# Kernel tuning notes

Measured on AMD Instinct MI355X. Metric: run time of the kernel, lower is better.

Reference implementation:

```python
import jax, jax.numpy as jnp
import numpy as np

N = 6144
DIN1, DIN2, DOUT, NUM_HEADS = 3000, 512, 64, 8


@jax.custom_vjp
def _ms(x):
    # multispike forward: floor(clamp(x, 0, 4) + 0.5)
    return jnp.floor(jnp.clip(x, 0.0, 4.0) + 0.5)


def _ms_fwd(x):
    return _ms(x), x


def _ms_bwd(x, g):
    # surrogate gradient: pass-through on 0 < x < lens(=4)
    return (g * ((x > 0) & (x < 4)).astype(g.dtype),)


_ms.defvjp(_ms_fwd, _ms_bwd)


def spike(x):
    # Multispike module: spike(4*x)/4
    return _ms(4.0 * x) * 0.25


def _attn(x, wq, wk, wv, wp):
    # SpikeAttention: linear attention kv = k^T v, out = q @ kv * 0.25
    n, c = x.shape
    d = c // NUM_HEADS
    xs = spike(x)
    q = spike(xs @ wq).reshape(n, NUM_HEADS, d)
    k = spike(xs @ wk).reshape(n, NUM_HEADS, d)
    v = spike(xs @ wv).reshape(n, NUM_HEADS, d)
    kv = jnp.einsum('nhd,nhe->hde', k, v)          # [H, d, d]
    o = jnp.einsum('nhd,hde->nhe', q, kv) * 0.25    # [N, H, d]
    return o.reshape(n, c) @ wp


def _encoder(feat, adj, w, wq, wk, wv, wp):
    fe = feat @ w                 # feat embedding [N, DOUT]
    x = spike(adj @ fe)           # aggregate + spike
    return x + _attn(x, wq, wk, wv, wp)


def _decoder(emb, adj, w):
    return spike(adj @ (emb @ w))


def _xavier(k, shp):
    lim = float(np.sqrt(6.0 / (shp[0] + shp[1])))
    return jax.random.uniform(k, shp, jnp.float32, -lim, lim)


def setup_inputs() -> dict:
    key = jax.random.key(0)
    ks = jax.random.split(key, 26)
    inp = {}
    inp['features_omics1'] = jax.random.normal(ks[0], (N, DIN1), jnp.float32)
    inp['features_omics2'] = jax.random.normal(ks[1], (N, DIN2), jnp.float32)
    # dense normalized-ish adjacencies: entries ~ U(0, 2/N) so row sums ~ 1
    for i, nm in enumerate(['adj_spatial_omics1', 'adj_feature_omics1',
                            'adj_spatial_omics2', 'adj_feature_omics2']):
        inp[nm] = jax.random.uniform(ks[2 + i], (N, N), jnp.float32) * (2.0 / N)
    # 1x1 conv (Conv2dLSQ approximated as plain conv): weight [2], bias [1]
    inp['conv1_w'] = jax.random.normal(ks[6], (2,), jnp.float32) * 0.5
    inp['conv1_b'] = jnp.zeros((1,), jnp.float32)
    inp['conv2_w'] = jax.random.normal(ks[7], (2,), jnp.float32) * 0.5
    inp['conv2_b'] = jnp.zeros((1,), jnp.float32)
    inp['w_enc1'] = _xavier(ks[8], (DIN1, DOUT))
    inp['wq1'] = _xavier(ks[9], (DOUT, DOUT))
    inp['wk1'] = _xavier(ks[10], (DOUT, DOUT))
    inp['wv1'] = _xavier(ks[11], (DOUT, DOUT))
    inp['wp1'] = _xavier(ks[12], (DOUT, DOUT))
    inp['w_enc2'] = _xavier(ks[13], (DIN2, DOUT))
    inp['wq2'] = _xavier(ks[14], (DOUT, DOUT))
    inp['wk2'] = _xavier(ks[15], (DOUT, DOUT))
    inp['wv2'] = _xavier(ks[16], (DOUT, DOUT))
    inp['wp2'] = _xavier(ks[17], (DOUT, DOUT))
    inp['fc1_w'] = _xavier(ks[18], (2 * DOUT, DOUT))
    inp['fc1_b'] = jnp.zeros((DOUT,), jnp.float32)
    inp['fc2_w'] = _xavier(ks[19], (DOUT, DOUT))
    inp['fc2_b'] = jnp.zeros((DOUT,), jnp.float32)
    inp['w_dec1'] = _xavier(ks[20], (DOUT, DIN1))
    inp['w_dec2'] = _xavier(ks[21], (DOUT, DIN2))
    return inp


def reference(features_omics1, features_omics2,
              adj_spatial_omics1, adj_feature_omics1,
              adj_spatial_omics2, adj_feature_omics2,
              conv1_w, conv1_b, conv2_w, conv2_b,
              w_enc1, wq1, wk1, wv1, wp1,
              w_enc2, wq2, wk2, wv2, wp2,
              fc1_w, fc1_b, fc2_w, fc2_b,
              w_dec1, w_dec2):
    # 1x1 conv over 2-channel stacked adjacencies -> weighted sum + bias
    af1 = conv1_w[0] * adj_spatial_omics1 + conv1_w[1] * adj_feature_omics1 + conv1_b[0]
    af2 = conv2_w[0] * adj_spatial_omics2 + conv2_w[1] * adj_feature_omics2 + conv2_b[0]
    emb1 = _encoder(features_omics1, af1, w_enc1, wq1, wk1, wv1, wp1)
    emb2 = _encoder(features_omics2, af2, w_enc2, wq2, wk2, wv2, wp2)
    cat = jnp.concatenate([emb1, emb2], axis=1)        # [N, 2*DOUT]
    comb = spike(cat @ fc1_w + fc1_b) @ fc2_w + fc2_b   # EnhancedMLP
    recon1 = _decoder(comb, adj_spatial_omics1, w_dec1)
    recon2 = _decoder(comb, adj_spatial_omics2, w_dec2)
    return (emb1, emb2, spike(comb), recon1, recon2)
```

## Files before the change

kernel.cpp:

```cpp
#include <hip/hip_runtime.h>

#define NROWS 6144
#define DIN1 3000
#define DIN2 512

typedef __attribute__((ext_vector_type(8))) short short8;
typedef __attribute__((ext_vector_type(4))) float floatx4;

__device__ __forceinline__ float spikef(float y) {
    float t = 4.0f * y;
    t = fminf(fmaxf(t, 0.0f), 4.0f);
    return floorf(t + 0.5f) * 0.25f;
}

__device__ __forceinline__ unsigned short f2bf(float f) {
    union { float f; unsigned u; } c; c.f = f;
    unsigned r = c.u + 0x7fffu + ((c.u >> 16) & 1u);
    return (unsigned short)(r >> 16);
}

__device__ __forceinline__ void fma_outer(float (&acc)[4][4], const float4& a, const float4& b) {
    const float av[4] = {a.x, a.y, a.z, a.w};
    const float bv[4] = {b.x, b.y, b.z, b.w};
#pragma unroll
    for (int i = 0; i < 4; i++)
#pragma unroll
        for (int j = 0; j < 4; j++)
            acc[i][j] += av[i] * bv[j];
}

template <bool COMBINE>
__global__ __launch_bounds__(256) void gemm_bf16(
    const float* __restrict__ A1, const float* __restrict__ A1b,
    const float* __restrict__ A2, const float* __restrict__ cw,
    const unsigned short* __restrict__ Bt, float* __restrict__ P,
    int K, int lda, int kchunk, int ldb, size_t bank_stride)
{
    __shared__ __align__(16) unsigned short Asb[128][72];
    __shared__ __align__(16) unsigned short Bts[64][72];

    const float* A = COMBINE ? A1 : (blockIdx.z ? A1b : A1);
    float c0 = 1.f, c1 = 0.f;
    if (COMBINE) { c0 = cw[0]; c1 = cw[1]; }

    int t = threadIdx.x;
    int r0 = blockIdx.x * 128;
    int s = blockIdx.y;
    int k0 = s * kchunk;
    int kend = min(K, k0 + kchunk);

    int w = t >> 6, lane = t & 63, quad = lane >> 4, l15 = lane & 15;
    int ar = t >> 4, ak = (t & 15) * 4;
    int bn = t >> 2, bk = (t & 3) * 16;

    floatx4 zf = {0.f, 0.f, 0.f, 0.f};
    floatx4 acc[2][4];
#pragma unroll
    for (int m = 0; m < 2; m++)
#pragma unroll
        for (int c = 0; c < 4; c++) acc[m][c] = zf;

    for (int kb = k0; kb < kend; kb += 64) {
        __syncthreads();
        *(uint4*)&Bts[bn][bk]     = *(const uint4*)&Bt[(size_t)bn * ldb + kb + bk];
        *(uint4*)&Bts[bn][bk + 8] = *(const uint4*)&Bt[(size_t)bn * ldb + kb + bk + 8];
#pragma unroll
        for (int p = 0; p < 8; p++) {
            int row = p * 16 + ar;
            int k = kb + ak;
            const float* ap = A + (size_t)(r0 + row) * lda;
            float4 v = make_float4(0.f, 0.f, 0.f, 0.f);
            if (k + 4 <= kend) {
                v = *(const float4*)(ap + k);
            } else if (k < kend) {
                float* vp = (float*)&v;
                for (int j = 0; j < 4; j++)
                    if (k + j < kend) vp[j] = ap[k + j];
            }
            if (COMBINE) {
                const float* ap2 = A2 + (size_t)(r0 + row) * lda;
                float4 v2 = make_float4(0.f, 0.f, 0.f, 0.f);
                if (k + 4 <= kend) {
                    v2 = *(const float4*)(ap2 + k);
                } else if (k < kend) {
                    float* vp = (float*)&v2;
                    for (int j = 0; j < 4; j++)
                        if (k + j < kend) vp[j] = ap2[k + j];
                }
                v.x = c0 * v.x + c1 * v2.x;
                v.y = c0 * v.y + c1 * v2.y;
                v.z = c0 * v.z + c1 * v2.z;
                v.w = c0 * v.w + c1 * v2.w;
            }
            unsigned lo = (unsigned)f2bf(v.x) | ((unsigned)f2bf(v.y) << 16);
            unsigned hi = (unsigned)f2bf(v.z) | ((unsigned)f2bf(v.w) << 16);
            *(uint2*)&Asb[row][ak] = make_uint2(lo, hi);
        }
        __syncthreads();
#pragma unroll
        for (int ks = 0; ks < 2; ks++) {
            short8 a0 = *(const short8*)&Asb[w * 32 + l15][ks * 32 + quad * 8];
            short8 a1 = *(const short8*)&Asb[w * 32 + 16 + l15][ks * 32 + quad * 8];
#pragma unroll
            for (int c = 0; c < 4; c++) {
                short8 b = *(const short8*)&Bts[c * 16 + l15][ks * 32 + quad * 8];
                acc[0][c] = __builtin_amdgcn_mfma_f32_16x16x32_bf16(a0, b, acc[0][c], 0, 0, 0);
                acc[1][c] = __builtin_amdgcn_mfma_f32_16x16x32_bf16(a1, b, acc[1][c], 0, 0, 0);
            }
        }
    }

    float* Pp = P + (size_t)blockIdx.z * bank_stride + ((size_t)s * NROWS + r0) * 64;
#pragma unroll
    for (int m = 0; m < 2; m++)
#pragma unroll
        for (int c = 0; c < 4; c++)
#pragma unroll
            for (int j = 0; j < 4; j++) {
                int row = w * 32 + m * 16 + quad * 4 + j;
                Pp[(size_t)row * 64 + c * 16 + l15] = acc[m][c][j];
            }
}

__global__ __launch_bounds__(256) void cvt_wT(const float* __restrict__ W,
                                              unsigned short* __restrict__ out,
                                              int K, int ldb)
{
    int kk = blockIdx.x * 64 + (threadIdx.x & 63);
    int ng = threadIdx.x >> 6;
    for (int n = ng; n < 64; n += 4)
        out[(size_t)n * ldb + kk] = (kk < K) ? f2bf(W[(size_t)kk * 64 + n]) : (unsigned short)0;
}

__global__ __launch_bounds__(256) void tcvt(const float* __restrict__ in,
                                            unsigned short* __restrict__ out)
{
    int r0 = blockIdx.x * 64;
    int k = threadIdx.x & 63;
    int ng = threadIdx.x >> 6;
    for (int n = ng; n < 64; n += 4)
        out[(size_t)n * NROWS + r0 + k] = f2bf(in[(size_t)(r0 + k) * 64 + n]);
}

__global__ __launch_bounds__(256) void reduce_p(
    const float* __restrict__ P, float* __restrict__ out,
    const float* __restrict__ colsum, const float* __restrict__ cb,
    int S, int spike_flag, size_t bank_stride)
{
    const float* Pz = P + (size_t)blockIdx.z * bank_stride;
    size_t idx = (size_t)blockIdx.x * 256 + threadIdx.x;
    float v = 0.f;
    for (int s = 0; s < S; s++) v += Pz[(size_t)s * NROWS * 64 + idx];
    if (colsum) v += cb[0] * colsum[idx & 63];
    if (spike_flag) v = spikef(v);
    out[(size_t)blockIdx.z * NROWS * 64 + idx] = v;
}

__global__ __launch_bounds__(256) void colsum_part(
    const float* __restrict__ fe1, const float* __restrict__ fe2,
    float* __restrict__ part)
{
    const float* fe = blockIdx.z ? fe2 : fe1;
    int r0 = blockIdx.x * 64;
    int g = threadIdx.x >> 6, j = threadIdx.x & 63;
    float v = 0.f;
    for (int i = g; i < 64; i += 4) v += fe[(size_t)(r0 + i) * 64 + j];
    __shared__ float red[4][64];
    red[g][j] = v;
    __syncthreads();
    if (g == 0)
        part[((size_t)blockIdx.z * 96 + blockIdx.x) * 64 + j] =
            red[0][j] + red[1][j] + red[2][j] + red[3][j];
}

__global__ __launch_bounds__(128) void colsum_final(const float* __restrict__ part,
                                                    float* __restrict__ colsum)
{
    int z = threadIdx.x >> 6, j = threadIdx.x & 63;
    float v = 0.f;
    for (int b = 0; b < 96; b++) v += part[((size_t)z * 96 + b) * 64 + j];
    colsum[z * 64 + j] = v;
}

__global__ __launch_bounds__(256) void qkv_kernel(
    const float* __restrict__ x, const float* __restrict__ wq,
    const float* __restrict__ wk, const float* __restrict__ wv,
    float* __restrict__ qo, float* __restrict__ ko, float* __restrict__ vo)
{
    __shared__ __align__(16) float xt[64 * 64];
    __shared__ __align__(16) float wqs[64 * 64];
    __shared__ __align__(16) float wks[64 * 64];
    __shared__ __align__(16) float wvs[64 * 64];
    int tid = threadIdx.x;
    int r0 = blockIdx.x * 64;
#pragma unroll
    for (int i = 0; i < 4; i++) {
        int qd = tid + i * 256;
        int row = qd >> 4, cq = (qd & 15) * 4;
        float4 xv = *(const float4*)(x + (size_t)(r0 + row) * 64 + cq);
        xt[(cq + 0) * 64 + row] = xv.x;
        xt[(cq + 1) * 64 + row] = xv.y;
        xt[(cq + 2) * 64 + row] = xv.z;
        xt[(cq + 3) * 64 + row] = xv.w;
        *(float4*)&wqs[qd * 4] = *(const float4*)(wq + (size_t)qd * 4);
        *(float4*)&wks[qd * 4] = *(const float4*)(wk + (size_t)qd * 4);
        *(float4*)&wvs[qd * 4] = *(const float4*)(wv + (size_t)qd * 4);
    }
    __syncthreads();
    int ty = tid >> 4, tx = tid & 15;
    float aq[4][4] = {}, ak[4][4] = {}, av[4][4] = {};
    for (int kk = 0; kk < 64; kk++) {
        float4 a = *(const float4*)&xt[kk * 64 + 4 * ty];
        float4 bq = *(const float4*)&wqs[kk * 64 + 4 * tx];
        float4 bk = *(const float4*)&wks[kk * 64 + 4 * tx];
        float4 bv = *(const float4*)&wvs[kk * 64 + 4 * tx];
        fma_outer(aq, a, bq);
        fma_outer(ak, a, bk);
        fma_outer(av, a, bv);
    }
#pragma unroll
    for (int i = 0; i < 4; i++) {
        size_t off = (size_t)(r0 + 4 * ty + i) * 64 + 4 * tx;
        float4 oq, ok, ov;
        oq.x = spikef(aq[i][0]); oq.y = spikef(aq[i][1]); oq.z = spikef(aq[i][2]); oq.w = spikef(aq[i][3]);
        ok.x = spikef(ak[i][0]); ok.y = spikef(ak[i][1]); ok.z = spikef(ak[i][2]); ok.w = spikef(ak[i][3]);
        ov.x = spikef(av[i][0]); ov.y = spikef(av[i][1]); ov.z = spikef(av[i][2]); ov.w = spikef(av[i][3]);
        *(float4*)(qo + off) = oq;
        *(float4*)(ko + off) = ok;
        *(float4*)(vo + off) = ov;
    }
}

__global__ __launch_bounds__(256) void kv_part_kernel(
    const float* __restrict__ k, const float* __restrict__ v, float* __restrict__ kvp)
{
    __shared__ __align__(16) float ks[64 * 64];
    __shared__ __align__(16) float vs[64 * 64];
    int tid = threadIdx.x;
    int r0 = blockIdx.x * 64;
#pragma unroll
    for (int i = 0; i < 4; i++) {
        int qd = tid + i * 256;
        int row = qd >> 4, cq = (qd & 15) * 4;
        *(float4*)&ks[qd * 4] = *(const float4*)(k + (size_t)(r0 + row) * 64 + cq);
        *(float4*)&vs[qd * 4] = *(const float4*)(v + (size_t)(r0 + row) * 64 + cq);
    }
    __syncthreads();
#pragma unroll
    for (int i = 0; i < 2; i++) {
        int ci = tid + i * 256;
        int h = ci >> 6, d = (ci >> 3) & 7, e = ci & 7;
        float acc = 0.f;
        for (int n = 0; n < 64; n++)
            acc += ks[n * 64 + h * 8 + d] * vs[n * 64 + h * 8 + e];
        kvp[(size_t)blockIdx.x * 512 + ci] = acc;
    }
}

__global__ __launch_bounds__(256) void attn_final(
    const float* __restrict__ q, const float* __restrict__ kvp,
    const float* __restrict__ wp, const float* __restrict__ x,
    float* __restrict__ emb)
{
    __shared__ __align__(16) float qs[64 * 64];
    __shared__ __align__(16) float ot[64 * 64];
    __shared__ __align__(16) float wps[64 * 64];
    __shared__ __align__(16) float kvs[512];
    int tid = threadIdx.x;
    int r0 = blockIdx.x * 64;
#pragma unroll
    for (int i = 0; i < 2; i++) {
        int ci = tid + i * 256;
        float vsum = 0.f;
        for (int ch = 0; ch < 96; ch++) vsum += kvp[(size_t)ch * 512 + ci];
        kvs[ci] = vsum;
    }
#pragma unroll
    for (int i = 0; i < 4; i++) {
        int qd = tid + i * 256;
        int row = qd >> 4, cq = (qd & 15) * 4;
        *(float4*)&qs[qd * 4] = *(const float4*)(q + (size_t)(r0 + row) * 64 + cq);
        *(float4*)&wps[qd * 4] = *(const float4*)(wp + (size_t)qd * 4);
    }
    __syncthreads();
    int ty = tid >> 4, tx = tid & 15;
    float o[4][4];
#pragma unroll
    for (int i = 0; i < 4; i++)
#pragma unroll
        for (int j = 0; j < 4; j++) {
            int r = 4 * ty + i, c = 4 * tx + j;
            int h = c >> 3, e = c & 7;
            float acc = 0.f;
#pragma unroll
            for (int d = 0; d < 8; d++)
                acc += qs[r * 64 + h * 8 + d] * kvs[h * 64 + d * 8 + e];
            o[i][j] = acc * 0.25f;
        }
#pragma unroll
    for (int i = 0; i < 4; i++)
#pragma unroll
        for (int j = 0; j < 4; j++)
            ot[(4 * tx + j) * 64 + (4 * ty + i)] = o[i][j];
    __syncthreads();
    float acc2[4][4] = {};
    for (int c = 0; c < 64; c++) {
        float4 a = *(const float4*)&ot[c * 64 + 4 * ty];
        float4 b = *(const float4*)&wps[c * 64 + 4 * tx];
        fma_outer(acc2, a, b);
    }
#pragma unroll
    for (int i = 0; i < 4; i++) {
        size_t off = (size_t)(r0 + 4 * ty + i) * 64 + 4 * tx;
        float4 xv = *(const float4*)(x + off);
        float4 ov;
        ov.x = xv.x + acc2[i][0];
        ov.y = xv.y + acc2[i][1];
        ov.z = xv.z + acc2[i][2];
        ov.w = xv.w + acc2[i][3];
        *(float4*)(emb + off) = ov;
    }
}

__global__ __launch_bounds__(256) void comb_kernel(
    const float* __restrict__ emb1, const float* __restrict__ emb2,
    const float* __restrict__ fc1w, const float* __restrict__ fc1b,
    const float* __restrict__ fc2w, const float* __restrict__ fc2b,
    float* __restrict__ comb, float* __restrict__ scomb)
{
    __shared__ __align__(16) float ct[128 * 64];
    __shared__ __align__(16) float fs[128 * 64];
    int tid = threadIdx.x;
    int r0 = blockIdx.x * 64;
#pragma unroll
    for (int i = 0; i < 4; i++) {
        int qd = tid + i * 256;
        int row = qd >> 4, cq = (qd & 15) * 4;
        float4 e1 = *(const float4*)(emb1 + (size_t)(r0 + row) * 64 + cq);
        float4 e2 = *(const float4*)(emb2 + (size_t)(r0 + row) * 64 + cq);
        ct[(cq + 0) * 64 + row] = e1.x;
        ct[(cq + 1) * 64 + row] = e1.y;
        ct[(cq + 2) * 64 + row] = e1.z;
        ct[(cq + 3) * 64 + row] = e1.w;
        ct[(64 + cq + 0) * 64 + row] = e2.x;
        ct[(64 + cq + 1) * 64 + row] = e2.y;
        ct[(64 + cq + 2) * 64 + row] = e2.z;
        ct[(64 + cq + 3) * 64 + row] = e2.w;
    }
#pragma unroll
    for (int i = 0; i < 8; i++) {
        int qd = tid + i * 256;
        *(float4*)&fs[qd * 4] = *(const float4*)(fc1w + (size_t)qd * 4);
    }
    __syncthreads();
    int ty = tid >> 4, tx = tid & 15;
    float acc[4][4] = {};
    for (int kk = 0; kk < 128; kk++) {
        float4 a = *(const float4*)&ct[kk * 64 + 4 * ty];
        float4 b = *(const float4*)&fs[kk * 64 + 4 * tx];
        fma_outer(acc, a, b);
    }
    float h[4][4];
#pragma unroll
    for (int j = 0; j < 4; j++) {
        float b1 = fc1b[4 * tx + j];
#pragma unroll
        for (int i = 0; i < 4; i++) h[i][j] = spikef(acc[i][j] + b1);
    }
    __syncthreads();
#pragma unroll
    for (int i = 0; i < 4; i++)
#pragma unroll
        for (int j = 0; j < 4; j++)
            ct[(4 * tx + j) * 64 + (4 * ty + i)] = h[i][j];
#pragma unroll
    for (int i = 0; i < 4; i++) {
        int qd = tid + i * 256;
        *(float4*)&fs[qd * 4] = *(const float4*)(fc2w + (size_t)qd * 4);
    }
    __syncthreads();
    float a2[4][4] = {};
    for (int c = 0; c < 64; c++) {
        float4 a = *(const float4*)&ct[c * 64 + 4 * ty];
        float4 b = *(const float4*)&fs[c * 64 + 4 * tx];
        fma_outer(a2, a, b);
    }
#pragma unroll
    for (int i = 0; i < 4; i++) {
        size_t off = (size_t)(r0 + 4 * ty + i) * 64 + 4 * tx;
        float4 cv, sv;
        float b20 = fc2b[4 * tx + 0], b21 = fc2b[4 * tx + 1];
        float b22 = fc2b[4 * tx + 2], b23 = fc2b[4 * tx + 3];
        cv.x = a2[i][0] + b20; cv.y = a2[i][1] + b21;
        cv.z = a2[i][2] + b22; cv.w = a2[i][3] + b23;
        sv.x = spikef(cv.x); sv.y = spikef(cv.y); sv.z = spikef(cv.z); sv.w = spikef(cv.w);
        *(float4*)(comb + off) = cv;
        *(float4*)(scomb + off) = sv;
    }
}

__global__ __launch_bounds__(256) void recon_kernel(
    const float* __restrict__ g, const float* __restrict__ W,
    float* __restrict__ out, int KO)
{
    __shared__ __align__(16) float gt[64 * 64];
    __shared__ __align__(16) float wsh[64 * 128];
    int tid = threadIdx.x;
    int r0 = blockIdx.x * 64;
    int c0 = blockIdx.y * 128;
#pragma unroll
    for (int i = 0; i < 4; i++) {
        int qd = tid + i * 256;
        int row = qd >> 4, cq = (qd & 15) * 4;
        float4 gv = *(const float4*)(g + (size_t)(r0 + row) * 64 + cq);
        gt[(cq + 0) * 64 + row] = gv.x;
        gt[(cq + 1) * 64 + row] = gv.y;
        gt[(cq + 2) * 64 + row] = gv.z;
        gt[(cq + 3) * 64 + row] = gv.w;
    }
#pragma unroll
    for (int i = 0; i < 8; i++) {
        int qd = tid + i * 256;
        int row = qd >> 5, cq = (qd & 31) * 4;
        float4 wv = make_float4(0.f, 0.f, 0.f, 0.f);
        if (c0 + cq + 4 <= KO) wv = *(const float4*)(W + (size_t)row * KO + c0 + cq);
        *(float4*)&wsh[row * 128 + cq] = wv;
    }
    __syncthreads();
    int ty = tid >> 5, tx = tid & 31;
    float accA[4][4] = {};
    float accB[4][4] = {};
    for (int kk = 0; kk < 64; kk++) {
        float4 a0 = *(const float4*)&gt[kk * 64 + 8 * ty];
        float4 a1 = *(const float4*)&gt[kk * 64 + 8 * ty + 4];
        float4 b = *(const float4*)&wsh[kk * 128 + 4 * tx];
        fma_outer(accA, a0, b);
        fma_outer(accB, a1, b);
    }
    if (c0 + 4 * tx < KO) {
#pragma unroll
        for (int i = 0; i < 8; i++) {
            int r = r0 + 8 * ty + i;
            const float (&ac)[4] = (i < 4) ? accA[i] : accB[i - 4];
            float4 ov;
            ov.x = spikef(ac[0]); ov.y = spikef(ac[1]);
            ov.z = spikef(ac[2]); ov.w = spikef(ac[3]);
            *(float4*)(out + (size_t)r * KO + c0 + 4 * tx) = ov;
        }
    }
}

extern "C" void kernel_launch(void* const* d_in, const int* in_sizes, int n_in,
                              void* d_out, int out_size, void* d_ws, size_t ws_size,
                              hipStream_t stream)
{
    (void)in_sizes; (void)n_in; (void)out_size; (void)ws_size;

    const float* F1    = (const float*)d_in[0];
    const float* F2    = (const float*)d_in[1];
    const float* Asp1  = (const float*)d_in[2];
    const float* Aft1  = (const float*)d_in[3];
    const float* Asp2  = (const float*)d_in[4];
    const float* Aft2  = (const float*)d_in[5];
    const float* c1w   = (const float*)d_in[6];
    const float* c1b   = (const float*)d_in[7];
    const float* c2w   = (const float*)d_in[8];
    const float* c2b   = (const float*)d_in[9];
    const float* Wenc1 = (const float*)d_in[10];
    const float* Wq1   = (const float*)d_in[11];
    const float* Wk1   = (const float*)d_in[12];
    const float* Wv1   = (const float*)d_in[13];
    const float* Wp1   = (const float*)d_in[14];
    const float* Wenc2 = (const float*)d_in[15];
    const float* Wq2   = (const float*)d_in[16];
    const float* Wk2   = (const float*)d_in[17];
    const float* Wv2   = (const float*)d_in[18];
    const float* Wp2   = (const float*)d_in[19];
    const float* FC1w  = (const float*)d_in[20];
    const float* FC1b  = (const float*)d_in[21];
    const float* FC2w  = (const float*)d_in[22];
    const float* FC2b  = (const float*)d_in[23];
    const float* Wd1   = (const float*)d_in[24];
    const float* Wd2   = (const float*)d_in[25];

    float* out = (float*)d_out;
    const size_t NC = (size_t)NROWS * 64;
    float* emb1  = out;
    float* emb2  = out + NC;
    float* scomb = out + 2 * NC;
    float* rec1  = out + 3 * NC;
    float* rec2  = out + 3 * NC + (size_t)NROWS * DIN1;

    float* ws   = (float*)d_ws;
    float* fe1  = ws;
    float* fe2  = ws + NC;
    float* x1   = ws + 2 * NC;
    float* x2   = ws + 3 * NC;
    float* qb   = ws + 4 * NC;
    float* kb   = ws + 5 * NC;
    float* vb   = ws + 6 * NC;
    float* comb = ws + 7 * NC;
    float* g    = ws + 8 * NC;
    float* csp  = ws + 10 * NC;
    float* csum = csp + 2 * 96 * 64;
    float* kvp  = csum + 128;
    float* P    = kvp + 96 * 512;
    const size_t PBANK = 8 * NC;
    unsigned short* WT1   = (unsigned short*)(P + 16 * NC);
    unsigned short* WT2   = WT1 + (size_t)64 * 3008;
    unsigned short* feT1  = WT2 + (size_t)64 * 512;
    unsigned short* feT2  = feT1 + (size_t)64 * NROWS;
    unsigned short* combT = feT2 + (size_t)64 * NROWS;

    cvt_wT<<<dim3(47, 1, 1), 256, 0, stream>>>(Wenc1, WT1, DIN1, 3008);
    cvt_wT<<<dim3(8, 1, 1), 256, 0, stream>>>(Wenc2, WT2, DIN2, 512);

    gemm_bf16<false><<<dim3(48, 16, 1), 256, 0, stream>>>(
        F1, F1, nullptr, nullptr, WT1, P, DIN1, DIN1, 192, 3008, 0);
    reduce_p<<<dim3(1536, 1, 1), 256, 0, stream>>>(P, fe1, nullptr, nullptr, 16, 0, 0);
    gemm_bf16<false><<<dim3(48, 8, 1), 256, 0, stream>>>(
        F2, F2, nullptr, nullptr, WT2, P, DIN2, DIN2, 64, 512, 0);
    reduce_p<<<dim3(1536, 1, 1), 256, 0, stream>>>(P, fe2, nullptr, nullptr, 8, 0, 0);
    colsum_part<<<dim3(96, 1, 2), 256, 0, stream>>>(fe1, fe2, csp);
    colsum_final<<<dim3(1, 1, 1), 128, 0, stream>>>(csp, csum);
    tcvt<<<dim3(96, 1, 1), 256, 0, stream>>>(fe1, feT1);
    tcvt<<<dim3(96, 1, 1), 256, 0, stream>>>(fe2, feT2);

    gemm_bf16<true><<<dim3(48, 16, 1), 256, 0, stream>>>(
        Asp1, Asp1, Aft1, c1w, feT1, P, NROWS, NROWS, 384, NROWS, 0);
    reduce_p<<<dim3(1536, 1, 1), 256, 0, stream>>>(P, x1, csum, c1b, 16, 1, 0);
    qkv_kernel<<<96, 256, 0, stream>>>(x1, Wq1, Wk1, Wv1, qb, kb, vb);
    kv_part_kernel<<<96, 256, 0, stream>>>(kb, vb, kvp);
    attn_final<<<96, 256, 0, stream>>>(qb, kvp, Wp1, x1, emb1);

    gemm_bf16<true><<<dim3(48, 16, 1), 256, 0, stream>>>(
        Asp2, Asp2, Aft2, c2w, feT2, P, NROWS, NROWS, 384, NROWS, 0);
    reduce_p<<<dim3(1536, 1, 1), 256, 0, stream>>>(P, x2, csum + 64, c2b, 16, 1, 0);
    qkv_kernel<<<96, 256, 0, stream>>>(x2, Wq2, Wk2, Wv2, qb, kb, vb);
    kv_part_kernel<<<96, 256, 0, stream>>>(kb, vb, kvp);
    attn_final<<<96, 256, 0, stream>>>(qb, kvp, Wp2, x2, emb2);

    comb_kernel<<<96, 256, 0, stream>>>(emb1, emb2, FC1w, FC1b, FC2w, FC2b, comb, scomb);
    tcvt<<<dim3(96, 1, 1), 256, 0, stream>>>(comb, combT);

    gemm_bf16<false><<<dim3(48, 8, 2), 256, 0, stream>>>(
        Asp1, Asp2, nullptr, nullptr, combT, P, NROWS, NROWS, 768, NROWS, PBANK);
    reduce_p<<<dim3(1536, 1, 2), 256, 0, stream>>>(P, g, nullptr, nullptr, 8, 0, PBANK);
    recon_kernel<<<dim3(96, 24, 1), 256, 0, stream>>>(g, Wd1, rec1, DIN1);
    recon_kernel<<<dim3(96, 4, 1), 256, 0, stream>>>(g + NC, Wd2, rec2, DIN2);
}
```

Measured before the change: 924.3 us.

## Halve GEMM row tile and issue global loads before the barrier

The bf16 MFMA GEMM row tile drops from 128 to 64 rows, so each wave computes one 16-row strip, and the grids double to match. Each thread now loads its A (and second A for the combine case) and B slices into registers before the first barrier, then converts and stores to LDS afterward. This overlaps global-load latency with other waves' compute. It also adds a launch bound of 4 blocks per CU to raise occupancy. The cost is less B-tile reuse per block and more register use for the staged values.

```diff
diff --git a/kernel.cpp b/kernel.cpp
--- a/kernel.cpp
+++ b/kernel.cpp
@@ -13,10 +13,10 @@
     return floorf(t + 0.5f) * 0.25f;
 }
 
-__device__ __forceinline__ unsigned short f2bf(float f) {
+__device__ __forceinline__ unsigned f2bf(float f) {
     union { float f; unsigned u; } c; c.f = f;
     unsigned r = c.u + 0x7fffu + ((c.u >> 16) & 1u);
-    return (unsigned short)(r >> 16);
+    return r >> 16;
 }
 
 __device__ __forceinline__ void fma_outer(float (&acc)[4][4], const float4& a, const float4& b) {
@@ -29,97 +29,103 @@
             acc[i][j] += av[i] * bv[j];
 }
 
-template <bool COMBINE>
-__global__ __launch_bounds__(256) void gemm_bf16(
+template <bool DUAL>
+__global__ __launch_bounds__(256, 4) void gemm_bf16(
     const float* __restrict__ A1, const float* __restrict__ A1b,
     const float* __restrict__ A2, const float* __restrict__ cw,
     const unsigned short* __restrict__ Bt, float* __restrict__ P,
     int K, int lda, int kchunk, int ldb, size_t bank_stride)
 {
-    __shared__ __align__(16) unsigned short Asb[128][72];
+    __shared__ __align__(16) unsigned short Asb[64][72];
     __shared__ __align__(16) unsigned short Bts[64][72];
 
-    const float* A = COMBINE ? A1 : (blockIdx.z ? A1b : A1);
+    const float* A = DUAL ? A1 : (blockIdx.z ? A1b : A1);
     float c0 = 1.f, c1 = 0.f;
-    if (COMBINE) { c0 = cw[0]; c1 = cw[1]; }
+    if (DUAL) { c0 = cw[0]; c1 = cw[1]; }
 
     int t = threadIdx.x;
-    int r0 = blockIdx.x * 128;
+    int r0 = blockIdx.x * 64;
     int s = blockIdx.y;
     int k0 = s * kchunk;
     int kend = min(K, k0 + kchunk);
 
     int w = t >> 6, lane = t & 63, quad = lane >> 4, l15 = lane & 15;
-    int ar = t >> 4, ak = (t & 15) * 4;
-    int bn = t >> 2, bk = (t & 3) * 16;
+    int ar = t >> 2, akq = (t & 3) * 16;
+
+    const float* apA = A + (size_t)(r0 + ar) * lda;
+    const float* apB = DUAL ? (A2 + (size_t)(r0 + ar) * lda) : apA;
+    const unsigned short* bp = Bt + (size_t)ar * ldb;
 
     floatx4 zf = {0.f, 0.f, 0.f, 0.f};
-    floatx4 acc[2][4];
-#pragma unroll
-    for (int m = 0; m < 2; m++)
-#pragma unroll
-        for (int c = 0; c < 4; c++) acc[m][c] = zf;
+    floatx4 acc[4];
+#pragma unroll
+    for (int c = 0; c < 4; c++) acc[c] = zf;
 
     for (int kb = k0; kb < kend; kb += 64) {
-        __syncthreads();
-        *(uint4*)&Bts[bn][bk]     = *(const uint4*)&Bt[(size_t)bn * ldb + kb + bk];
-        *(uint4*)&Bts[bn][bk + 8] = *(const uint4*)&Bt[(size_t)bn * ldb + kb + bk + 8];
-#pragma unroll
-        for (int p = 0; p < 8; p++) {
-            int row = p * 16 + ar;
-            int k = kb + ak;
-            const float* ap = A + (size_t)(r0 + row) * lda;
+        uint4 bv0 = *(const uint4*)(bp + kb + akq);
+        uint4 bv1 = *(const uint4*)(bp + kb + akq + 8);
+        float4 va[4], vb[4];
+#pragma unroll
+        for (int j = 0; j < 4; j++) {
+            int k = kb + akq + j * 4;
             float4 v = make_float4(0.f, 0.f, 0.f, 0.f);
             if (k + 4 <= kend) {
-                v = *(const float4*)(ap + k);
+                v = *(const float4*)(apA + k);
             } else if (k < kend) {
                 float* vp = (float*)&v;
-                for (int j = 0; j < 4; j++)
-                    if (k + j < kend) vp[j] = ap[k + j];
+                for (int q = 0; q < 4; q++)
+                    if (k + q < kend) vp[q] = apA[k + q];
             }
-            if (COMBINE) {
-                const float* ap2 = A2 + (size_t)(r0 + row) * lda;
-                float4 v2 = make_float4(0.f, 0.f, 0.f, 0.f);
+            va[j] = v;
+            if (DUAL) {
+                float4 u = make_float4(0.f, 0.f, 0.f, 0.f);
                 if (k + 4 <= kend) {
-                    v2 = *(const float4*)(ap2 + k);
+                    u = *(const float4*)(apB + k);
                 } else if (k < kend) {
-                    float* vp = (float*)&v2;
-                    for (int j = 0; j < 4; j++)
-                        if (k + j < kend) vp[j] = ap2[k + j];
+                    float* up = (float*)&u;
+                    for (int q = 0; q < 4; q++)
+                        if (k + q < kend) up[q] = apB[k + q];
                 }
-                v.x = c0 * v.x + c1 * v2.x;
-                v.y = c0 * v.y + c1 * v2.y;
-                v.z = c0 * v.z + c1 * v2.z;
-                v.w = c0 * v.w + c1 * v2.w;
+                vb[j] = u;
             }
-            unsigned lo = (unsigned)f2bf(v.x) | ((unsigned)f2bf(v.y) << 16);
-            unsigned hi = (unsigned)f2bf(v.z) | ((unsigned)f2bf(v.w) << 16);
-            *(uint2*)&Asb[row][ak] = make_uint2(lo, hi);
         }
         __syncthreads();
 #pragma unroll
+        for (int j = 0; j < 4; j++) {
+            float4 v = va[j];
+            if (DUAL) {
+                float4 u = vb[j];
+                v.x = c0 * v.x + c1 * u.x;
+                v.y = c0 * v.y + c1 * u.y;
+                v.z = c0 * v.z + c1 * u.z;
+                v.w = c0 * v.w + c1 * u.w;
+            }
+            unsigned lo = f2bf(v.x) | (f2bf(v.y) << 16);
+            unsigned hi = f2bf(v.z) | (f2bf(v.w) << 16);
+            *(uint2*)&Asb[ar][akq + j * 4] = make_uint2(lo, hi);
+        }
+        *(uint4*)&Bts[ar][akq] = bv0;
+        *(uint4*)&Bts[ar][akq + 8] = bv1;
+        __syncthreads();
+#pragma unroll
         for (int ks = 0; ks < 2; ks++) {
-            short8 a0 = *(const short8*)&Asb[w * 32 + l15][ks * 32 + quad * 8];
-            short8 a1 = *(const short8*)&Asb[w * 32 + 16 + l15][ks * 32 + quad * 8];
+            short8 a = *(const short8*)&Asb[w * 16 + l15][ks * 32 + quad * 8];
 #pragma unroll
             for (int c = 0; c < 4; c++) {
                 short8 b = *(const short8*)&Bts[c * 16 + l15][ks * 32 + quad * 8];
-                acc[0][c] = __builtin_amdgcn_mfma_f32_16x16x32_bf16(a0, b, acc[0][c], 0, 0, 0);
-                acc[1][c] = __builtin_amdgcn_mfma_f32_16x16x32_bf16(a1, b, acc[1][c], 0, 0, 0);
+                acc[c] = __builtin_amdgcn_mfma_f32_16x16x32_bf16(a, b, acc[c], 0, 0, 0);
             }
         }
     }
 
     float* Pp = P + (size_t)blockIdx.z * bank_stride + ((size_t)s * NROWS + r0) * 64;
 #pragma unroll
-    for (int m = 0; m < 2; m++)
-#pragma unroll
-        for (int c = 0; c < 4; c++)
-#pragma unroll
-            for (int j = 0; j < 4; j++) {
-                int row = w * 32 + m * 16 + quad * 4 + j;
-                Pp[(size_t)row * 64 + c * 16 + l15] = acc[m][c][j];
-            }
+    for (int c = 0; c < 4; c++)
+#pragma unroll
+        for (int j = 0; j < 4; j++) {
+            int row = w * 16 + quad * 4 + j;
+            Pp[(size_t)row * 64 + c * 16 + l15] = acc[c][j];
+        }
 }
 
 __global__ __launch_bounds__(256) void cvt_wT(const float* __restrict__ W,
@@ -129,7 +135,8 @@
     int kk = blockIdx.x * 64 + (threadIdx.x & 63);
     int ng = threadIdx.x >> 6;
     for (int n = ng; n < 64; n += 4)
-        out[(size_t)n * ldb + kk] = (kk < K) ? f2bf(W[(size_t)kk * 64 + n]) : (unsigned short)0;
+        out[(size_t)n * ldb + kk] = (kk < K) ? (unsigned short)f2bf(W[(size_t)kk * 64 + n])
+                                             : (unsigned short)0;
 }
 
 __global__ __launch_bounds__(256) void tcvt(const float* __restrict__ in,
@@ -139,7 +146,7 @@
     int k = threadIdx.x & 63;
     int ng = threadIdx.x >> 6;
     for (int n = ng; n < 64; n += 4)
-        out[(size_t)n * NROWS + r0 + k] = f2bf(in[(size_t)(r0 + k) * 64 + n]);
+        out[(size_t)n * NROWS + r0 + k] = (unsigned short)f2bf(in[(size_t)(r0 + k) * 64 + n]);
 }
 
 __global__ __launch_bounds__(256) void reduce_p(
@@ -515,10 +522,10 @@
     cvt_wT<<<dim3(47, 1, 1), 256, 0, stream>>>(Wenc1, WT1, DIN1, 3008);
     cvt_wT<<<dim3(8, 1, 1), 256, 0, stream>>>(Wenc2, WT2, DIN2, 512);
 
-    gemm_bf16<false><<<dim3(48, 16, 1), 256, 0, stream>>>(
+    gemm_bf16<false><<<dim3(96, 16, 1), 256, 0, stream>>>(
         F1, F1, nullptr, nullptr, WT1, P, DIN1, DIN1, 192, 3008, 0);
     reduce_p<<<dim3(1536, 1, 1), 256, 0, stream>>>(P, fe1, nullptr, nullptr, 16, 0, 0);
-    gemm_bf16<false><<<dim3(48, 8, 1), 256, 0, stream>>>(
+    gemm_bf16<false><<<dim3(96, 8, 1), 256, 0, stream>>>(
         F2, F2, nullptr, nullptr, WT2, P, DIN2, DIN2, 64, 512, 0);
     reduce_p<<<dim3(1536, 1, 1), 256, 0, stream>>>(P, fe2, nullptr, nullptr, 8, 0, 0);
     colsum_part<<<dim3(96, 1, 2), 256, 0, stream>>>(fe1, fe2, csp);
@@ -526,14 +533,14 @@
     tcvt<<<dim3(96, 1, 1), 256, 0, stream>>>(fe1, feT1);
     tcvt<<<dim3(96, 1, 1), 256, 0, stream>>>(fe2, feT2);
 
-    gemm_bf16<true><<<dim3(48, 16, 1), 256, 0, stream>>>(
+    gemm_bf16<true><<<dim3(96, 16, 1), 256, 0, stream>>>(
         Asp1, Asp1, Aft1, c1w, feT1, P, NROWS, NROWS, 384, NROWS, 0);
     reduce_p<<<dim3(1536, 1, 1), 256, 0, stream>>>(P, x1, csum, c1b, 16, 1, 0);
     qkv_kernel<<<96, 256, 0, stream>>>(x1, Wq1, Wk1, Wv1, qb, kb, vb);
     kv_part_kernel<<<96, 256, 0, stream>>>(kb, vb, kvp);
     attn_final<<<96, 256, 0, stream>>>(qb, kvp, Wp1, x1, emb1);
 
-    gemm_bf16<true><<<dim3(48, 16, 1), 256, 0, stream>>>(
+    gemm_bf16<true><<<dim3(96, 16, 1), 256, 0, stream>>>(
         Asp2, Asp2, Aft2, c2w, feT2, P, NROWS, NROWS, 384, NROWS, 0);
     reduce_p<<<dim3(1536, 1, 1), 256, 0, stream>>>(P, x2, csum + 64, c2b, 16, 1, 0);
     qkv_kernel<<<96, 256, 0, stream>>>(x2, Wq2, Wk2, Wv2, qb, kb, vb);
@@ -543,7 +550,7 @@
     comb_kernel<<<96, 256, 0, stream>>>(emb1, emb2, FC1w, FC1b, FC2w, FC2b, comb, scomb);
     tcvt<<<dim3(96, 1, 1), 256, 0, stream>>>(comb, combT);
 
-    gemm_bf16<false><<<dim3(48, 8, 2), 256, 0, stream>>>(
+    gemm_bf16<false><<<dim3(96, 8, 2), 256, 0, stream>>>(
         Asp1, Asp2, nullptr, nullptr, combT, P, NROWS, NROWS, 768, NROWS, PBANK);
     reduce_p<<<dim3(1536, 1, 2), 256, 0, stream>>>(P, g, nullptr, nullptr, 8, 0, PBANK);
     recon_kernel<<<dim3(96, 24, 1), 256, 0, stream>>>(g, Wd1, rec1, DIN1);
```

After: 1.069 ms. +15.6%, slower.
